# Optimization experiments

Measured on AMD Instinct MI355X. Metric: run time of the kernel, lower is better.

The kernel has to match this reference:

```python
import jax, jax.numpy as jnp
import numpy as np

B, T, F, D = 8, 2048, 512, 256

def setup_inputs() -> dict:
    key = jax.random.key(0)
    k1, k2, k3, k4 = jax.random.split(key, 4)
    scale = 1.0 / np.sqrt(F)
    return {
        "inputs": jax.random.normal(k1, (B, T, F), dtype=jnp.float32),
        "W_q": jax.random.normal(k2, (F, D), dtype=jnp.float32) * scale,
        "W_k": jax.random.normal(k3, (F, D), dtype=jnp.float32) * scale,
        "W_v": jax.random.normal(k4, (F, D), dtype=jnp.float32) * scale,
    }

def reference(inputs, W_q, W_k, W_v):
    # Q,K,V: [B,T,D]
    Q = jnp.einsum('btf,fd->btd', inputs, W_q)
    K = jnp.einsum('btf,fd->btd', inputs, W_k)
    V = jnp.einsum('btf,fd->btd', inputs, W_v)
    d = Q.shape[-1]
    scores = jnp.einsum('bqd,bkd->bqk', Q, K) / jnp.sqrt(jnp.asarray(d, dtype=Q.dtype))
    attn = jax.nn.softmax(scores, axis=-1)  # [B,T,T]
    return jnp.einsum('bqk,bkd->bqd', attn, V)
```

## Files before the change

kernel.cpp:

```cpp
#include <hip/hip_runtime.h>
#include <cstdint>
#include <cstddef>

#define B_ 8
#define T_ 2048
#define F_ 512
#define D_ 256
#define NSPLIT 2
#define KVB 32
#define NT ((T_ / NSPLIT) / KVB)

typedef float f32x4 __attribute__((ext_vector_type(4)));
typedef __bf16 bf16x8 __attribute__((ext_vector_type(8)));
typedef unsigned short us8 __attribute__((ext_vector_type(8)));
typedef unsigned short us4 __attribute__((ext_vector_type(4)));

static __device__ __forceinline__ unsigned short f2bf(float f) {
  union { float f; unsigned int u; } v; v.f = f;
  unsigned int u = v.u;
  u += 0x7fffu + ((u >> 16) & 1u);
  return (unsigned short)(u >> 16);
}

static __device__ __forceinline__ float bf2f(unsigned short s) {
  union { float f; unsigned int u; } v; v.u = ((unsigned int)s) << 16;
  return v.f;
}

static __device__ __forceinline__ bf16x8 ldb8(const unsigned short* p) {
  return *reinterpret_cast<const bf16x8*>(p);
}

static __device__ __forceinline__ f32x4 mfma_bf16(bf16x8 a, bf16x8 b, f32x4 c) {
  return __builtin_amdgcn_mfma_f32_16x16x32_bf16(a, b, c, 0, 0, 0);
}

static __device__ __forceinline__ void gload_lds16(const unsigned short* g,
                                                   unsigned short* l) {
  __builtin_amdgcn_global_load_lds(
      (const __attribute__((address_space(1))) void*)g,
      (__attribute__((address_space(3))) void*)l, 16, 0, 0);
}

__global__ __launch_bounds__(256) void xb_kernel(const float* __restrict__ X,
                                                 unsigned short* __restrict__ Xb) {
  size_t i = ((size_t)blockIdx.x * 256 + threadIdx.x) * 8;
  float4 a = *reinterpret_cast<const float4*>(&X[i]);
  float4 b = *reinterpret_cast<const float4*>(&X[i + 4]);
  us8 p;
  p[0] = f2bf(a.x); p[1] = f2bf(a.y); p[2] = f2bf(a.z); p[3] = f2bf(a.w);
  p[4] = f2bf(b.x); p[5] = f2bf(b.y); p[6] = f2bf(b.z); p[7] = f2bf(b.w);
  *reinterpret_cast<us8*>(&Xb[i]) = p;
}

__global__ __launch_bounds__(256) void tw_kernel(const float* __restrict__ Wq,
                                                 const float* __restrict__ Wk,
                                                 const float* __restrict__ Wv,
                                                 unsigned short* __restrict__ Wt) {
  __shared__ unsigned short tile[64][72];
  const float* W = (blockIdx.z == 0) ? Wq : (blockIdx.z == 1) ? Wk : Wv;
  unsigned short* out = Wt + (size_t)blockIdx.z * (D_ * F_);
  int k0 = blockIdx.x * 64, n0 = blockIdx.y * 64;
  int t = threadIdx.x;
#pragma unroll
  for (int i = 0; i < 4; i++) {
    int c = t + 256 * i;
    int r = c >> 4, c4 = (c & 15) * 4;
    float4 v = *reinterpret_cast<const float4*>(&W[(size_t)(k0 + r) * D_ + n0 + c4]);
    us4 p; p[0] = f2bf(v.x); p[1] = f2bf(v.y); p[2] = f2bf(v.z); p[3] = f2bf(v.w);
    *reinterpret_cast<us4*>(&tile[r][c4]) = p;
  }
  __syncthreads();
#pragma unroll
  for (int i = 0; i < 4; i++) {
    int c = t + 256 * i;
    int r = c >> 4, c4 = (c & 15) * 4;
    us4 p;
    p[0] = tile[c4 + 0][r];
    p[1] = tile[c4 + 1][r];
    p[2] = tile[c4 + 2][r];
    p[3] = tile[c4 + 3][r];
    *reinterpret_cast<us4*>(&out[(size_t)(n0 + r) * F_ + k0 + c4]) = p;
  }
}

__global__ __launch_bounds__(256) void proj_kernel(const unsigned short* __restrict__ Xb,
                                                   const unsigned short* __restrict__ Wt,
                                                   unsigned short* __restrict__ Qs,
                                                   unsigned short* __restrict__ Kb,
                                                   unsigned short* __restrict__ Vt) {
  __shared__ unsigned short Au[2][128 * 64];
  __shared__ unsigned short Bu[2][128 * 64];
  const int brow = blockIdx.x * 128;
  const int bcol = blockIdx.y * 128;
  const int z = blockIdx.z;
  const unsigned short* W = Wt + (size_t)z * (D_ * F_);
  const int tid = threadIdx.x;
  const int wave = tid >> 6, lane = tid & 63;
  const int wr = wave >> 1, wc = wave & 1;
  const int lg = lane >> 4, lr = lane & 15;

  f32x4 acc[4][4] = {};

  auto stageT = [&](unsigned short* dst, const unsigned short* srcBase, int k0) {
#pragma unroll
    for (int i = 0; i < 4; i++) {
      int L = (tid + 256 * i) * 16;
      int r = L >> 7;
      int c = L & 127;
      int csw = c ^ ((r & 7) << 4);
      gload_lds16(srcBase + (size_t)r * F_ + k0 + (csw >> 1), dst + (L >> 1));
    }
  };

  stageT(Au[0], Xb + (size_t)brow * F_, 0);
  stageT(Bu[0], W + (size_t)bcol * F_, 0);
  __syncthreads();

  for (int ks = 0; ks < 8; ks++) {
    const int cur = ks & 1;
    if (ks + 1 < 8) {
      stageT(Au[cur ^ 1], Xb + (size_t)brow * F_, (ks + 1) * 64);
      stageT(Bu[cur ^ 1], W + (size_t)bcol * F_, (ks + 1) * 64);
    }
#pragma unroll
    for (int kk = 0; kk < 2; kk++) {
      bf16x8 af[4], bfr[4];
#pragma unroll
      for (int mi = 0; mi < 4; mi++) {
        int r = wr * 64 + mi * 16 + lr;
        af[mi] = ldb8(&Au[cur][r * 64 + ((((kk * 64 + lg * 16) ^ ((r & 7) << 4))) >> 1)]);
      }
#pragma unroll
      for (int ni = 0; ni < 4; ni++) {
        int r = wc * 64 + ni * 16 + lr;
        bfr[ni] = ldb8(&Bu[cur][r * 64 + ((((kk * 64 + lg * 16) ^ ((r & 7) << 4))) >> 1)]);
      }
#pragma unroll
      for (int mi = 0; mi < 4; mi++)
#pragma unroll
        for (int ni = 0; ni < 4; ni++)
          acc[mi][ni] = mfma_bf16(af[mi], bfr[ni], acc[mi][ni]);
    }
    __syncthreads();
  }

#pragma unroll
  for (int mi = 0; mi < 4; mi++) {
#pragma unroll
    for (int ni = 0; ni < 4; ni++) {
      int row0 = brow + wr * 64 + mi * 16 + lg * 4;
      int col = bcol + wc * 64 + ni * 16 + lr;
      if (z == 0) {
#pragma unroll
        for (int j = 0; j < 4; j++)
          Qs[(size_t)(row0 + j) * D_ + col] = f2bf(acc[mi][ni][j] * 0.09016844f);
      } else if (z == 1) {
#pragma unroll
        for (int j = 0; j < 4; j++)
          Kb[(size_t)(row0 + j) * D_ + col] = f2bf(acc[mi][ni][j]);
      } else {
        int b = row0 >> 11, t0 = row0 & (T_ - 1);
        us4 p;
#pragma unroll
        for (int j = 0; j < 4; j++) p[j] = f2bf(acc[mi][ni][j]);
        *reinterpret_cast<us4*>(&Vt[(size_t)b * D_ * T_ + (size_t)col * T_ + t0]) = p;
      }
    }
  }
}

__global__ __launch_bounds__(256)
void flash_kernel(const unsigned short* __restrict__ Qs,
                  const unsigned short* __restrict__ Kb,
                  const unsigned short* __restrict__ Vt,
                  unsigned short* __restrict__ op,
                  float2* __restrict__ ml) {
  __shared__ unsigned short Kl[2][KVB * 256];
  __shared__ unsigned short Vl[2][256 * KVB];
  __shared__ unsigned short Pl[4][16][40];

  const int b = blockIdx.x, qt = blockIdx.y, h = blockIdx.z;
  const int tid = threadIdx.x;
  const int wave = tid >> 6, lane = tid & 63;
  const int lg = lane >> 4, lr = lane & 15;

  const int qrow = qt * 64 + wave * 16 + lr;
  const unsigned short* qptr = Qs + ((size_t)b * T_ + qrow) * D_;
  bf16x8 qf[8];
#pragma unroll
  for (int ks = 0; ks < 8; ks++) qf[ks] = ldb8(qptr + ks * 32 + lg * 8);

  f32x4 o[16] = {};
  float m = -__builtin_inff();
  float lsum = 0.f;

  const int keyoff = h * (T_ / NSPLIT);
  const unsigned short* kbase = Kb + (size_t)b * T_ * D_ + (size_t)keyoff * D_;
  const unsigned short* vbase = Vt + (size_t)b * D_ * T_;

  auto stage = [&](int buf, int kt) {
    const unsigned short* ksrc = kbase + (size_t)kt * KVB * D_;
#pragma unroll
    for (int i = 0; i < 4; i++) {
      int L = (tid + 256 * i) * 16;
      int r = L >> 9;
      int c = L & 511;
      int csw = c ^ ((r & 7) << 4);
      gload_lds16(ksrc + r * 256 + (csw >> 1), &Kl[buf][L >> 1]);
    }
    const int key0 = keyoff + kt * KVB;
#pragma unroll
    for (int i = 0; i < 4; i++) {
      int L = (tid + 256 * i) * 16;
      int d = L >> 6;
      int c = L & 63;
      int csw = c ^ (((d >> 1) & 3) << 4);
      gload_lds16(vbase + (size_t)d * T_ + key0 + (csw >> 1), &Vl[buf][L >> 1]);
    }
  };

  stage(0, 0);
  __syncthreads();

  for (int kt = 0; kt < NT; kt++) {
    const int cur = kt & 1;
    if (kt + 1 < NT) stage(cur ^ 1, kt + 1);

    f32x4 s[2] = {};
    __builtin_amdgcn_s_setprio(1);
#pragma unroll
    for (int ks = 0; ks < 8; ks++) {
#pragma unroll
      for (int nf = 0; nf < 2; nf++) {
        int r = nf * 16 + lr;
        bf16x8 kb = ldb8(&Kl[cur][r * 256 + (((ks * 64 + lg * 16) ^ ((r & 7) << 4)) >> 1)]);
        s[nf] = mfma_bf16(kb, qf[ks], s[nf]);
      }
    }
    __builtin_amdgcn_s_setprio(0);

    float pm;
    {
      float a0 = fmaxf(fmaxf(s[0][0], s[0][1]), fmaxf(s[0][2], s[0][3]));
      float a1 = fmaxf(fmaxf(s[1][0], s[1][1]), fmaxf(s[1][2], s[1][3]));
      pm = fmaxf(a0, a1);
      pm = fmaxf(pm, __shfl_xor(pm, 16));
      pm = fmaxf(pm, __shfl_xor(pm, 32));
    }
    if (!__all(pm - m <= 11.5f)) {
      float mn = fmaxf(m, pm);
      float corr = exp2f(m - mn);
      m = mn;
      lsum *= corr;
#pragma unroll
      for (int nf = 0; nf < 16; nf++)
#pragma unroll
        for (int j = 0; j < 4; j++) o[nf][j] *= corr;
    }
    float rs = 0.f;
#pragma unroll
    for (int nf = 0; nf < 2; nf++) {
      us4 pk;
#pragma unroll
      for (int j = 0; j < 4; j++) {
        float p = exp2f(s[nf][j] - m);
        rs += p;
        pk[j] = f2bf(p);
      }
      *reinterpret_cast<us4*>(&Pl[wave][lr][nf * 16 + lg * 4]) = pk;
    }
    rs += __shfl_xor(rs, 16);
    rs += __shfl_xor(rs, 32);
    lsum += rs;

    __builtin_amdgcn_s_setprio(1);
    {
      bf16x8 pa = ldb8(&Pl[wave][lr][lg * 8]);
#pragma unroll
      for (int nf = 0; nf < 16; nf++) {
        int d = nf * 16 + lr;
        bf16x8 vb = ldb8(&Vl[cur][d * 32 + (((lg * 16) ^ (((d >> 1) & 3) << 4)) >> 1)]);
        o[nf] = mfma_bf16(vb, pa, o[nf]);
      }
    }
    __builtin_amdgcn_s_setprio(0);

    __syncthreads();
  }

  const size_t rowbase = (size_t)h * (B_ * T_) + (size_t)b * T_;
  const int q = qt * 64 + wave * 16 + lr;
#pragma unroll
  for (int nf = 0; nf < 16; nf++) {
    us4 st;
#pragma unroll
    for (int j = 0; j < 4; j++) st[j] = f2bf(o[nf][j]);
    *reinterpret_cast<us4*>(&op[(rowbase + q) * D_ + nf * 16 + lg * 4]) = st;
  }
  if (lg == 0) {
    ml[rowbase + q] = make_float2(m, lsum);
  }
}

__global__ __launch_bounds__(256) void merge_kernel(const unsigned short* __restrict__ op,
                                                    const float2* __restrict__ ml,
                                                    float* __restrict__ out) {
  const int tid = threadIdx.x;
  const int row = blockIdx.x * 4 + (tid >> 6);
  const int d0 = (tid & 63) * 4;

  float mh[NSPLIT], lh[NSPLIT];
  float M = -__builtin_inff();
#pragma unroll
  for (int hh = 0; hh < NSPLIT; hh++) {
    float2 v = ml[(size_t)hh * (B_ * T_) + row];
    mh[hh] = v.x; lh[hh] = v.y;
    M = fmaxf(M, v.x);
  }
  float e[NSPLIT], den = 0.f;
#pragma unroll
  for (int hh = 0; hh < NSPLIT; hh++) {
    e[hh] = exp2f(mh[hh] - M);
    den += e[hh] * lh[hh];
  }
  const float inv = 1.0f / den;

  float acc[4] = {0.f, 0.f, 0.f, 0.f};
#pragma unroll
  for (int hh = 0; hh < NSPLIT; hh++) {
    us4 p = *reinterpret_cast<const us4*>(
        &op[((size_t)hh * (B_ * T_) + row) * D_ + d0]);
#pragma unroll
    for (int j = 0; j < 4; j++) acc[j] += e[hh] * bf2f(p[j]);
  }
  float4 r;
  r.x = acc[0] * inv; r.y = acc[1] * inv; r.z = acc[2] * inv; r.w = acc[3] * inv;
  *reinterpret_cast<float4*>(&out[(size_t)row * D_ + d0]) = r;
}

extern "C" void kernel_launch(void* const* d_in, const int* in_sizes, int n_in,
                              void* d_out, int out_size, void* d_ws, size_t ws_size,
                              hipStream_t stream) {
  const float* X  = (const float*)d_in[0];
  const float* Wq = (const float*)d_in[1];
  const float* Wk = (const float*)d_in[2];
  const float* Wv = (const float*)d_in[3];
  float* out = (float*)d_out;

  char* ws = (char*)d_ws;
  unsigned short* Wt = (unsigned short*)ws;
  unsigned short* Qs = (unsigned short*)(ws + 786432);
  unsigned short* Kb = (unsigned short*)(ws + 786432 + 8388608);
  unsigned short* Vt = (unsigned short*)(ws + 786432 + 2 * 8388608);
  unsigned short* op = (unsigned short*)(ws + 786432 + 3 * 8388608);
  unsigned short* Xb = op;
  float2* ml        = (float2*)(ws + 786432 + 3 * 8388608 + (size_t)NSPLIT * B_ * T_ * D_ * 2);

  xb_kernel<<<dim3((B_ * T_ * F_) / (256 * 8)), 256, 0, stream>>>(X, Xb);
  tw_kernel<<<dim3(F_ / 64, D_ / 64, 3), 256, 0, stream>>>(Wq, Wk, Wv, Wt);
  proj_kernel<<<dim3((B_ * T_) / 128, D_ / 128, 3), 256, 0, stream>>>(Xb, Wt, Qs, Kb, Vt);
  flash_kernel<<<dim3(B_, T_ / 64, NSPLIT), 256, 0, stream>>>(Qs, Kb, Vt, op, ml);
  merge_kernel<<<dim3(B_ * T_ / 4), 256, 0, stream>>>(op, ml, out);
}
```

Before: 108.6 us.

## Feed softmax probabilities directly to 16x16x16 MFMA, removing LDS round trip

```diff
diff --git a/kernel.cpp b/kernel.cpp
--- a/kernel.cpp
+++ b/kernel.cpp
@@ -12,6 +12,7 @@
 
 typedef float f32x4 __attribute__((ext_vector_type(4)));
 typedef __bf16 bf16x8 __attribute__((ext_vector_type(8)));
+typedef short s16x4 __attribute__((ext_vector_type(4)));
 typedef unsigned short us8 __attribute__((ext_vector_type(8)));
 typedef unsigned short us4 __attribute__((ext_vector_type(4)));
 
@@ -33,6 +34,21 @@
 
 static __device__ __forceinline__ f32x4 mfma_bf16(bf16x8 a, bf16x8 b, f32x4 c) {
   return __builtin_amdgcn_mfma_f32_16x16x32_bf16(a, b, c, 0, 0, 0);
+}
+
+#if defined(__has_builtin)
+#if __has_builtin(__builtin_amdgcn_mfma_f32_16x16x16bf16_1k)
+#define HAVE_MFMA16 1
+#endif
+#endif
+static __device__ __forceinline__ f32x4 mfma16(us4 a, us4 b, f32x4 c) {
+#ifdef HAVE_MFMA16
+  return __builtin_amdgcn_mfma_f32_16x16x16bf16_1k((s16x4)a, (s16x4)b, c, 0, 0, 0);
+#else
+  asm volatile("v_mfma_f32_16x16x16_bf16 %0, %1, %2, %0"
+               : "+v"(c) : "v"(a), "v"(b));
+  return c;
+#endif
 }
 
 static __device__ __forceinline__ void gload_lds16(const unsigned short* g,
@@ -178,7 +194,6 @@
                   float2* __restrict__ ml) {
   __shared__ unsigned short Kl[2][KVB * 256];
   __shared__ unsigned short Vl[2][256 * KVB];
-  __shared__ unsigned short Pl[4][16][40];
 
   const int b = blockIdx.x, qt = blockIdx.y, h = blockIdx.z;
   const int tid = threadIdx.x;
@@ -258,36 +273,37 @@
 #pragma unroll
         for (int j = 0; j < 4; j++) o[nf][j] *= corr;
     }
-    float rs = 0.f;
-#pragma unroll
-    for (int nf = 0; nf < 2; nf++) {
-      us4 pk;
-#pragma unroll
-      for (int j = 0; j < 4; j++) {
-        float p = exp2f(s[nf][j] - m);
-        rs += p;
-        pk[j] = f2bf(p);
-      }
-      *reinterpret_cast<us4*>(&Pl[wave][lr][nf * 16 + lg * 4]) = pk;
-    }
-    rs += __shfl_xor(rs, 16);
-    rs += __shfl_xor(rs, 32);
-    lsum += rs;
+    union { __bf16 x[4]; us4 u; } pk0, pk1;
+#pragma unroll
+    for (int j = 0; j < 4; j++) {
+      float p0 = exp2f(s[0][j] - m);
+      float p1 = exp2f(s[1][j] - m);
+      lsum += p0 + p1;
+      pk0.x[j] = (__bf16)p0;
+      pk1.x[j] = (__bf16)p1;
+    }
 
     __builtin_amdgcn_s_setprio(1);
-    {
-      bf16x8 pa = ldb8(&Pl[wave][lr][lg * 8]);
-#pragma unroll
-      for (int nf = 0; nf < 16; nf++) {
-        int d = nf * 16 + lr;
-        bf16x8 vb = ldb8(&Vl[cur][d * 32 + (((lg * 16) ^ (((d >> 1) & 3) << 4)) >> 1)]);
-        o[nf] = mfma_bf16(vb, pa, o[nf]);
-      }
+#pragma unroll
+    for (int nf = 0; nf < 16; nf++) {
+      int d = nf * 16 + lr;
+      int swzd = ((d >> 1) & 3) << 4;
+      us4 va0 = *reinterpret_cast<const us4*>(&Vl[cur][d * 32 + (((lg * 8) ^ swzd) >> 1)]);
+      us4 va1 = *reinterpret_cast<const us4*>(&Vl[cur][d * 32 + (((32 + lg * 8) ^ swzd) >> 1)]);
+      o[nf] = mfma16(va0, pk0.u, o[nf]);
+      o[nf] = mfma16(va1, pk1.u, o[nf]);
     }
     __builtin_amdgcn_s_setprio(0);
 
     __syncthreads();
   }
+
+#ifndef HAVE_MFMA16
+  asm volatile("s_nop 7\n\ts_nop 7" ::: );
+#endif
+
+  lsum += __shfl_xor(lsum, 16);
+  lsum += __shfl_xor(lsum, 32);
 
   const size_t rowbase = (size_t)h * (B_ * T_) + (size_t)b * T_;
   const int q = qt * 64 + wave * 16 + lr;
```

Measured after the change: 118.9 us. 9.5% more time.
